# Kernel tuning notes

Hardware: AMD Instinct MI355X
Metric: run time of the kernel (lower is better)

## Reference

```python
import jax, jax.numpy as jnp
import numpy as np

B, R, C, H, W = 8, 4, 64, 128, 128
RF, E = 256, 8
C2 = 2 * C
K = 3


def setup_inputs() -> dict:
    key = jax.random.key(0)
    ks = jax.random.split(key, 8)
    return {
        "x": jax.random.normal(ks[0], (B, C, H, W), jnp.float32),
        "routing": jax.random.normal(ks[1], (B, R, RF), jnp.float32),
        # nn.Linear(routing_features, num_experts)
        "routing_W": jax.random.normal(ks[2], (RF, E), jnp.float32) * 0.05,
        "routing_b": jnp.zeros((E,), jnp.float32),
        # CondConv2d expert weights: (E, Cout, Cin, k, k)
        "W1": jax.random.normal(ks[3], (E, C2, C, K, K), jnp.float32) * 0.04,
        "prelu_a": jnp.float32(0.25),  # PReLU single shared parameter
        "W2": jax.random.normal(ks[4], (E, C, C2, K, K), jnp.float32) * 0.03,
        # self-routing Linear(2*in_features, num_experts)
        "sr_W": jax.random.normal(ks[5], (C2, E), jnp.float32) * 0.08,
        "sr_b": jnp.zeros((E,), jnp.float32),
        # conv_output: Conv2d(in_features, 1, kernel_size=1) with bias
        "Wout": jax.random.normal(ks[6], (1, C), jnp.float32) * 0.1,
        "bout": jnp.zeros((1,), jnp.float32),
    }


def _prelu(x, a):
    return jnp.where(x >= 0, x, a * x)


def _cond_conv(x, rw, Wexp):
    # x: (B,Cin,H,W); rw: (B,E); Wexp: (E,Cout,Cin,k,k)
    # per-sample mixed kernel, then per-sample conv (vmap over batch)
    w = jnp.einsum('be,eoikl->boikl', rw, Wexp)
    def one(xi, wi):
        return jax.lax.conv_general_dilated(
            xi[None], wi, window_strides=(1, 1), padding=[(1, 1), (1, 1)])[0]
    return jax.vmap(one)(x, w)


def reference(x, routing, routing_W, routing_b, W1, prelu_a, W2, sr_W, sr_b, Wout, bout):
    rw = jax.nn.sigmoid(routing @ routing_W + routing_b)  # (B,R,E)
    rw = jnp.transpose(rw, (1, 0, 2))                     # (R,B,E)

    def per_head(rw_r):
        xc = _prelu(_cond_conv(x, rw_r, W1), prelu_a)      # (B,C2,H,W)
        pooled = xc.mean(axis=(2, 3))                      # adaptive_avg_pool2d(.,1)
        srw = pooled @ sr_W + sr_b                         # no sigmoid (per source)
        xc2 = _prelu(_cond_conv(xc, srw, W2), prelu_a)     # (B,C,H,W)
        out = jnp.einsum('bchw,oc->bohw', xc2, Wout)       # 1x1 conv
        return out + bout[None, :, None, None]             # (B,1,H,W)

    res = jax.vmap(per_head)(rw)                           # (R,B,1,H,W)
    return jnp.transpose(res[:, :, 0], (1, 0, 2, 3))       # (B,R,H,W)
```

## Files before the change

### kernel.cpp

```cpp
#include <hip/hip_runtime.h>
#include <stdint.h>


typedef _Float16 f16_t;
typedef _Float16 f16x8 __attribute__((ext_vector_type(8)));
typedef _Float16 f16x4 __attribute__((ext_vector_type(4)));
typedef float    f32x4 __attribute__((ext_vector_type(4)));

#define B_   8
#define R_   4
#define C_   64
#define C2_  128
#define H_   128
#define W_   128
#define E_   8
#define RF_  256
#define WP_  130
#define HP_  130

__device__ __forceinline__ f32x4 mfma16(f16x8 a, f16x8 b, f32x4 c) {
  return __builtin_amdgcn_mfma_f32_16x16x32_f16(a, b, c, 0, 0, 0);
}

__device__ __forceinline__ void gl16(const f16_t* g, f16_t* l) {
  __builtin_amdgcn_global_load_lds(
      (const __attribute__((address_space(1))) unsigned int*)(const void*)g,
      (__attribute__((address_space(3))) unsigned int*)(void*)l, 16, 0, 0);
}

__device__ __host__ __forceinline__ int sig(int n) { return (n ^ (n >> 2)) & 3; }

__global__ void k_rw(const float* __restrict__ routing, const float* __restrict__ rW,
                     const float* __restrict__ rB, float* __restrict__ rw,
                     float* __restrict__ pooled4) {
  int t = threadIdx.x;
  #pragma unroll
  for (int i = 0; i < 16; ++i) pooled4[i*256 + t] = 0.f;
  int e = t & 7, b = (t >> 3) & 7, r = t >> 6;
  float acc = rB[e];
  for (int f = 0; f < RF_; ++f)
    acc += routing[(b*R_ + r)*RF_ + f] * rW[f*E_ + e];
  rw[(r*B_ + b)*E_ + e] = 1.0f / (1.0f + __expf(-acc));
}

__global__ void k_zero(f16_t* __restrict__ xbt, f16_t* __restrict__ xct) {
  const f16x8 z = {0,0,0,0,0,0,0,0};
  int t = blockIdx.x*256 + threadIdx.x;
  if (t < 16640) {
    int ch = t & 7, u = t >> 3;
    int pix = u % 130; u /= 130;
    int rs = u & 1, b = u >> 1;
    *(f16x8*)&xbt[((size_t)(b*HP_ + rs*129)*WP_ + pix)*C_ + ch*8] = z;
    return;
  }
  t -= 16640;
  if (t < 33280) {
    int ch = t & 15, u = t >> 4;
    int pix = u % 130; u /= 130;
    int rs = u & 1, b = u >> 1;
    *(f16x8*)&xct[((size_t)(b*HP_ + rs*129)*WP_ + pix)*C2_ + ch*8] = z;
    return;
  }
  t -= 33280;
  if (t < 32768) {
    int ch = t & 15, u = t >> 4;
    int hp = (u & 127) + 1; u >>= 7;
    int cs = u & 1, b = u >> 1;
    *(f16x8*)&xct[((size_t)(b*HP_ + hp)*WP_ + cs*129)*C2_ + ch*8] = z;
  }
}

__global__ void k_xt(const float* __restrict__ x, f16_t* __restrict__ xbt) {
  int wh = blockIdx.x, h = blockIdx.y, b = blockIdx.z;
  int t = threadIdx.x;
  int w0 = wh * 64;
  __shared__ float tile[64][65];
  #pragma unroll
  for (int rep = 0; rep < 16; ++rep) {
    int idx = rep*256 + t;
    int c = idx >> 6, w = idx & 63;
    tile[c][w] = x[((size_t)(b*C_ + c)*H_ + h)*W_ + w0 + w];
  }
  __syncthreads();
  #pragma unroll
  for (int rep = 0; rep < 16; ++rep) {
    int idx = rep*256 + t;
    int w = idx >> 6, c = idx & 63;
    xbt[((size_t)(b*HP_ + h + 1)*WP_ + (w0 + w + 1))*C_ + c] = (f16_t)tile[c][w];
  }
  if (t < 64) {
    if (wh == 0) xbt[((size_t)(b*HP_ + h + 1)*WP_ + 0)*C_ + t]   = (f16_t)0.0f;
    else         xbt[((size_t)(b*HP_ + h + 1)*WP_ + 129)*C_ + t] = (f16_t)0.0f;
  }
}

__global__ void k_mix1(const float* __restrict__ rw, const float* __restrict__ W1,
                       f16_t* __restrict__ w1m) {
  int gid = blockIdx.x*256 + threadIdx.x;
  int cq4 = gid & 15;
  int s   = (gid >> 4) % 9;
  int t2  = (gid >> 4) / 9;
  int co  = t2 & 127;
  int rb  = t2 >> 7;
  float o0=0.f,o1=0.f,o2=0.f,o3=0.f;
  #pragma unroll
  for (int e = 0; e < E_; ++e) {
    float rv = rw[rb*E_ + e];
    const float* wp = W1 + (size_t)((e*C2_ + co)*C_ + cq4*4)*9 + s;
    o0 += rv*wp[0]; o1 += rv*wp[9]; o2 += rv*wp[18]; o3 += rv*wp[27];
  }
  f16x4 pk; pk[0]=(f16_t)o0; pk[1]=(f16_t)o1; pk[2]=(f16_t)o2; pk[3]=(f16_t)o3;
  int coh = co >> 6, co6 = co & 63;
  int cb  = cq4 >> 3;
  int cqu = (cq4 >> 1) & 3;
  int off = (cq4 & 1) * 4;
  size_t row = ((size_t)(rb*2 + coh)*2 + cb)*64 + co6;
  *(f16x4*)&w1m[row*288 + (size_t)(s*4 + (cqu ^ sig(co6)))*8 + off] = pk;
}

__global__ void k_mix2(const float* __restrict__ pooled_r, const float* __restrict__ srW,
                       const float* __restrict__ srb, const float* __restrict__ W2,
                       f16_t* __restrict__ w2m) {
  __shared__ float sw[64];
  int t = threadIdx.x;
  if (t < 64) {
    int b = t >> 3, e = t & 7;
    float acc = srb[e];
    for (int c = 0; c < C2_; ++c)
      acc += pooled_r[b*C2_ + c] * (1.0f/16384.0f) * srW[c*E_ + e];
    sw[t] = acc;
  }
  __syncthreads();
  int gid = blockIdx.x*256 + t;
  int c2q = gid & 31;
  int s   = (gid >> 5) % 9;
  int t2  = (gid >> 5) / 9;
  int co  = t2 & 63;
  int b   = t2 >> 6;
  float o0=0.f,o1=0.f,o2=0.f,o3=0.f;
  #pragma unroll
  for (int e = 0; e < E_; ++e) {
    float rv = sw[b*E_ + e];
    const float* wp = W2 + (size_t)((e*C_ + co)*C2_ + c2q*4)*9 + s;
    o0 += rv*wp[0]; o1 += rv*wp[9]; o2 += rv*wp[18]; o3 += rv*wp[27];
  }
  f16x4 pk; pk[0]=(f16_t)o0; pk[1]=(f16_t)o1; pk[2]=(f16_t)o2; pk[3]=(f16_t)o3;
  int it  = c2q >> 3;
  int cqu = (c2q >> 1) & 3;
  int off = (c2q & 1) * 4;
  size_t row = ((size_t)b*4 + it)*64 + co;
  *(f16x4*)&w2m[row*288 + (size_t)(s*4 + (cqu ^ sig(co)))*8 + off] = pk;
}

__global__ __launch_bounds__(256, 2) void k_conv1(
    const f16_t* __restrict__ xbt, const f16_t* __restrict__ w1m,
    const float* __restrict__ pa, f16_t* __restrict__ xct,
    float* __restrict__ pooled_r, int r)
{
  const int bx = blockIdx.x;
  const int b = bx & 7, h0 = (bx >> 3) << 1;
  const int coh = blockIdx.y;
  const int tid = threadIdx.x;
  const int lane = tid & 63;
  const int wid = tid >> 6;
  const int wrow = wid >> 1, wph = wid & 1;
  const int l15 = lane & 15, l4 = lane >> 4;
  __shared__ __align__(16) f16_t lA[64*288];
  __shared__ __align__(16) f16_t lB[2080*8];

  const int xorA = (l4 ^ sig(l15)) << 4;
  int bbase[3];
  #pragma unroll
  for (int dw = 0; dw < 3; ++dw) {
    int P0 = wph*64 + dw + l15;
    bbase[dw] = P0*64 + ((l4 ^ sig(P0)) << 4);
  }

  const f32x4 vzero = {0.f,0.f,0.f,0.f};
  f32x4 acc[4][4];
  #pragma unroll
  for (int i=0;i<4;++i)
    #pragma unroll
    for (int j=0;j<4;++j) acc[i][j] = vzero;

  const int rb = r*B_ + b;
  const f16_t* w1base = w1m + ((size_t)(rb*2 + coh)*2)*64*288;
  const f16_t* xb = xbt + ((size_t)(b*HP_ + h0))*WP_*C_;

  for (int cb = 0; cb < 2; ++cb) {
    __syncthreads();
    #pragma unroll
    for (int k = 0; k < 9; ++k) {
      int u = k*256 + tid;
      gl16(w1base + (size_t)cb*64*288 + (size_t)u*8, &lA[u*8]);
    }
    #pragma unroll
    for (int k = 0; k < 8; ++k) {
      int u = k*256 + tid;
      int row = u / 520, rem = u - row*520;
      int pix = rem >> 2, cq = (rem & 3) ^ sig(pix);
      gl16(xb + ((size_t)row*WP_ + pix)*C_ + cb*32 + cq*8, &lB[u*8]);
    }
    if (tid < 32) {
      int u = 2048 + tid;
      int rem = u - 1560;
      int pix = rem >> 2, cq = (rem & 3) ^ sig(pix);
      gl16(xb + ((size_t)3*WP_ + pix)*C_ + cb*32 + cq*8, &lB[u*8]);
    }
    __syncthreads();
    __builtin_amdgcn_s_setprio(1);
    #pragma unroll
    for (int dh = 0; dh < 3; ++dh) {
      #pragma unroll
      for (int dw = 0; dw < 3; ++dw) {
        const int s = dh*3 + dw;
        f16x8 af[4], bf[4];
        #pragma unroll
        for (int fm = 0; fm < 4; ++fm)
          af[fm] = *(const f16x8*)((const char*)lA + (fm*16 + l15)*576 + s*64 + xorA);
        #pragma unroll
        for (int fn = 0; fn < 4; ++fn)
          bf[fn] = *(const f16x8*)((const char*)lB + (wrow + dh)*8320 + bbase[dw] + fn*1024);
        #pragma unroll
        for (int fm = 0; fm < 4; ++fm)
          #pragma unroll
          for (int fn = 0; fn < 4; ++fn)
            acc[fm][fn] = mfma16(af[fm], bf[fn], acc[fm][fn]);
      }
    }
    __builtin_amdgcn_s_setprio(0);
  }

  const float a = pa[0];
  float ps[4][4];
  #pragma unroll
  for (int fm=0;fm<4;++fm)
    #pragma unroll
    for (int j=0;j<4;++j) ps[fm][j] = 0.f;
  #pragma unroll
  for (int fm = 0; fm < 4; ++fm)
    #pragma unroll
    for (int fn = 0; fn < 4; ++fn)
      #pragma unroll
      for (int j = 0; j < 4; ++j) {
        float v = acc[fm][fn][j];
        v = (v >= 0.f) ? v : a*v;
        acc[fm][fn][j] = v;
        ps[fm][j] += v;
      }
  #pragma unroll
  for (int fm = 0; fm < 4; ++fm)
    #pragma unroll
    for (int j = 0; j < 4; ++j) {
      float s = ps[fm][j];
      s += __shfl_xor(s, 1, 64);
      s += __shfl_xor(s, 2, 64);
      s += __shfl_xor(s, 4, 64);
      s += __shfl_xor(s, 8, 64);
      ps[fm][j] = s;
    }
  __syncthreads();
  f16_t* lso = lA;
  float* lps = (float*)lB;
  const int prow = wrow*128 + wph*64;
  #pragma unroll
  for (int fm = 0; fm < 4; ++fm)
    #pragma unroll
    for (int fn = 0; fn < 4; ++fn) {
      f16x4 pk;
      #pragma unroll
      for (int j = 0; j < 4; ++j) pk[j] = (f16_t)acc[fm][fn][j];
      *(f16x4*)&lso[(prow + fn*16 + l15)*72 + fm*16 + l4*4] = pk;
    }
  if (l15 == 0) {
    #pragma unroll
    for (int fm = 0; fm < 4; ++fm)
      #pragma unroll
      for (int j = 0; j < 4; ++j)
        lps[wid*64 + fm*16 + l4*4 + j] = ps[fm][j];
  }
  __syncthreads();
  #pragma unroll
  for (int p = 0; p < 8; ++p) {
    int i = p*256 + tid;
    int pl = i >> 3, q = i & 7;
    int row = pl >> 7, pix = pl & 127;
    uint4 v = *(const uint4*)&lso[pl*72 + q*8];
    *(uint4*)(xct + ((size_t)(b*HP_ + h0 + row + 1)*WP_ + pix + 1)*C2_ + coh*64 + q*8) = v;
  }
  if (tid < 64) {
    float s = lps[tid] + lps[64 + tid] + lps[128 + tid] + lps[192 + tid];
    atomicAdd(&pooled_r[b*C2_ + coh*64 + tid], s);
  }
}

__global__ __launch_bounds__(256, 2) void k_conv2(
    const f16_t* __restrict__ xct, const f16_t* __restrict__ w2m,
    const float* __restrict__ pa, const float* __restrict__ Wout,
    const float* __restrict__ bout, float* __restrict__ out, int r)
{
  const int bx = blockIdx.x;
  const int b = bx & 7, h0 = (bx >> 3) << 1;
  const int tid = threadIdx.x;
  const int lane = tid & 63;
  const int wid = tid >> 6;
  const int wrow = wid >> 1, wph = wid & 1;
  const int l15 = lane & 15, l4 = lane >> 4;
  __shared__ __align__(16) f16_t lA[64*288];
  __shared__ __align__(16) f16_t lB[2080*8];

  const int xorA = (l4 ^ sig(l15)) << 4;
  int bbase[3];
  #pragma unroll
  for (int dw = 0; dw < 3; ++dw) {
    int P0 = wph*64 + dw + l15;
    bbase[dw] = P0*64 + ((l4 ^ sig(P0)) << 4);
  }

  const f32x4 vzero = {0.f,0.f,0.f,0.f};
  f32x4 acc[4][4];
  #pragma unroll
  for (int i=0;i<4;++i)
    #pragma unroll
    for (int j=0;j<4;++j) acc[i][j] = vzero;

  const f16_t* w2base = w2m + (size_t)b*4*64*288;
  const f16_t* xb = xct + ((size_t)(b*HP_ + h0))*WP_*C2_;

  for (int it = 0; it < 4; ++it) {
    __syncthreads();
    #pragma unroll
    for (int k = 0; k < 9; ++k) {
      int u = k*256 + tid;
      gl16(w2base + (size_t)it*64*288 + (size_t)u*8, &lA[u*8]);
    }
    #pragma unroll
    for (int k = 0; k < 8; ++k) {
      int u = k*256 + tid;
      int row = u / 520, rem = u - row*520;
      int pix = rem >> 2, cq = (rem & 3) ^ sig(pix);
      gl16(xb + ((size_t)row*WP_ + pix)*C2_ + it*32 + cq*8, &lB[u*8]);
    }
    if (tid < 32) {
      int u = 2048 + tid;
      int rem = u - 1560;
      int pix = rem >> 2, cq = (rem & 3) ^ sig(pix);
      gl16(xb + ((size_t)3*WP_ + pix)*C2_ + it*32 + cq*8, &lB[u*8]);
    }
    __syncthreads();
    __builtin_amdgcn_s_setprio(1);
    #pragma unroll
    for (int dh = 0; dh < 3; ++dh) {
      #pragma unroll
      for (int dw = 0; dw < 3; ++dw) {
        const int s = dh*3 + dw;
        f16x8 af[4], bf[4];
        #pragma unroll
        for (int fm = 0; fm < 4; ++fm)
          af[fm] = *(const f16x8*)((const char*)lA + (fm*16 + l15)*576 + s*64 + xorA);
        #pragma unroll
        for (int fn = 0; fn < 4; ++fn)
          bf[fn] = *(const f16x8*)((const char*)lB + (wrow + dh)*8320 + bbase[dw] + fn*1024);
        #pragma unroll
        for (int fm = 0; fm < 4; ++fm)
          #pragma unroll
          for (int fn = 0; fn < 4; ++fn)
            acc[fm][fn] = mfma16(af[fm], bf[fn], acc[fm][fn]);
      }
    }
    __builtin_amdgcn_s_setprio(0);
  }

  const float a  = pa[0];
  const float bo = bout[0];
  float wr_[4][4];
  #pragma unroll
  for (int fm = 0; fm < 4; ++fm)
    #pragma unroll
    for (int j = 0; j < 4; ++j)
      wr_[fm][j] = Wout[fm*16 + l4*4 + j];
  float* orow = out + ((size_t)((b*R_ + r)*H_ + h0 + wrow))*W_;
  #pragma unroll
  for (int fn = 0; fn < 4; ++fn) {
    float s = 0.f;
    #pragma unroll
    for (int fm = 0; fm < 4; ++fm)
      #pragma unroll
      for (int j = 0; j < 4; ++j) {
        float v = acc[fm][fn][j];
        v = (v >= 0.f) ? v : a*v;
        s += wr_[fm][j]*v;
      }
    s += __shfl_xor(s, 16, 64);
    s += __shfl_xor(s, 32, 64);
    if (lane < 16)
      orow[wph*64 + fn*16 + lane] = s + bo;
  }
}

extern "C" void kernel_launch(void* const* d_in, const int* in_sizes, int n_in,
                              void* d_out, int out_size, void* d_ws, size_t ws_size,
                              hipStream_t stream) {
  (void)in_sizes; (void)n_in; (void)out_size; (void)ws_size;
  const float* x       = (const float*)d_in[0];
  const float* routing = (const float*)d_in[1];
  const float* rW      = (const float*)d_in[2];
  const float* rB      = (const float*)d_in[3];
  const float* W1      = (const float*)d_in[4];
  const float* pa      = (const float*)d_in[5];
  const float* W2      = (const float*)d_in[6];
  const float* srW     = (const float*)d_in[7];
  const float* srb     = (const float*)d_in[8];
  const float* Wout    = (const float*)d_in[9];
  const float* bout    = (const float*)d_in[10];
  float* out = (float*)d_out;

  char* ws = (char*)d_ws;
  size_t off = 0;
  f16_t* xbt = (f16_t*)(ws + off); off += (size_t)B_*HP_*WP_*C_*2;
  f16_t* w1m = (f16_t*)(ws + off); off += (size_t)8192*288*2;
  f16_t* xct = (f16_t*)(ws + off); off += (size_t)B_*HP_*WP_*C2_*2;
  f16_t* w2m = (f16_t*)(ws + off); off += (size_t)2048*288*2;
  float* rw     = (float*)(ws + off); off += (size_t)R_*B_*E_*4;
  float* pooled = (float*)(ws + off); off += (size_t)R_*B_*C2_*4;

  k_rw  <<<1, 256, 0, stream>>>(routing, rW, rB, rw, pooled);
  k_zero<<<323, 256, 0, stream>>>(xbt, xct);
  k_xt  <<<dim3(2, H_, B_), 256, 0, stream>>>(x, xbt);
  k_mix1<<<2304, 256, 0, stream>>>(rw, W1, w1m);
  for (int r = 0; r < R_; ++r) {
    float* pooled_r = pooled + (size_t)r*B_*C2_;
    k_conv1<<<dim3(512, 2), 256, 0, stream>>>(xbt, w1m, pa, xct, pooled_r, r);
    k_mix2 <<<576, 256, 0, stream>>>(pooled_r, srW, srb, W2, w2m);
    k_conv2<<<dim3(512), 256, 0, stream>>>(xct, w2m, pa, Wout, bout, out, r);
  }
}
```

Baseline: 293.2 us.

## Batch the four routing heads into single conv and mix launches

The per-head loop of conv1, mix2 and conv2 launches is replaced by one launch of each kernel, with the head index taken from an extra grid dimension. Each head gets its own copy of the intermediate activation buffer and the mixed weight buffer, and the zero-padding kernel now clears the halos of all four copies. This aims to cut launch overhead and the serialization between heads, and to fill the GPU with more blocks at once. The cost is four times the intermediate workspace and more cache pressure. The code falls back to the old per-head loop if the workspace is too small.

Result: faster. 242.8 us (-17.2%).

```diff
diff --git a/kernel.cpp b/kernel.cpp
--- a/kernel.cpp
+++ b/kernel.cpp
@@ -43,7 +43,8 @@
   rw[(r*B_ + b)*E_ + e] = 1.0f / (1.0f + __expf(-acc));
 }
 
-__global__ void k_zero(f16_t* __restrict__ xbt, f16_t* __restrict__ xct) {
+__global__ void k_zero(f16_t* __restrict__ xbt, f16_t* __restrict__ xct,
+                       size_t xct_stride) {
   const f16x8 z = {0,0,0,0,0,0,0,0};
   int t = blockIdx.x*256 + threadIdx.x;
   if (t < 16640) {
@@ -54,19 +55,21 @@
     return;
   }
   t -= 16640;
-  if (t < 33280) {
+  if (t < 133120) {
     int ch = t & 15, u = t >> 4;
     int pix = u % 130; u /= 130;
-    int rs = u & 1, b = u >> 1;
-    *(f16x8*)&xct[((size_t)(b*HP_ + rs*129)*WP_ + pix)*C2_ + ch*8] = z;
+    int rs = u & 1; u >>= 1;
+    int b = u & 7, r = u >> 3;
+    *(f16x8*)&xct[(size_t)r*xct_stride + ((size_t)(b*HP_ + rs*129)*WP_ + pix)*C2_ + ch*8] = z;
     return;
   }
-  t -= 33280;
-  if (t < 32768) {
+  t -= 133120;
+  if (t < 131072) {
     int ch = t & 15, u = t >> 4;
     int hp = (u & 127) + 1; u >>= 7;
-    int cs = u & 1, b = u >> 1;
-    *(f16x8*)&xct[((size_t)(b*HP_ + hp)*WP_ + cs*129)*C2_ + ch*8] = z;
+    int cs = u & 1; u >>= 1;
+    int b = u & 7, r = u >> 3;
+    *(f16x8*)&xct[(size_t)r*xct_stride + ((size_t)(b*HP_ + hp)*WP_ + cs*129)*C2_ + ch*8] = z;
   }
 }
 
@@ -118,9 +121,12 @@
   *(f16x4*)&w1m[row*288 + (size_t)(s*4 + (cqu ^ sig(co6)))*8 + off] = pk;
 }
 
-__global__ void k_mix2(const float* __restrict__ pooled_r, const float* __restrict__ srW,
+__global__ void k_mix2(const float* __restrict__ pooled, const float* __restrict__ srW,
                        const float* __restrict__ srb, const float* __restrict__ W2,
-                       f16_t* __restrict__ w2m) {
+                       f16_t* __restrict__ w2m, size_t w2m_stride, int r0) {
+  const int r = r0 + blockIdx.y;
+  const float* pooled_r = pooled + (size_t)r*B_*C2_;
+  f16_t* w2m_r = w2m + (size_t)r*w2m_stride;
   __shared__ float sw[64];
   int t = threadIdx.x;
   if (t < 64) {
@@ -149,17 +155,20 @@
   int cqu = (c2q >> 1) & 3;
   int off = (c2q & 1) * 4;
   size_t row = ((size_t)b*4 + it)*64 + co;
-  *(f16x4*)&w2m[row*288 + (size_t)(s*4 + (cqu ^ sig(co)))*8 + off] = pk;
+  *(f16x4*)&w2m_r[row*288 + (size_t)(s*4 + (cqu ^ sig(co)))*8 + off] = pk;
 }
 
 __global__ __launch_bounds__(256, 2) void k_conv1(
     const f16_t* __restrict__ xbt, const f16_t* __restrict__ w1m,
-    const float* __restrict__ pa, f16_t* __restrict__ xct,
-    float* __restrict__ pooled_r, int r)
+    const float* __restrict__ pa, f16_t* __restrict__ xct, size_t xct_stride,
+    float* __restrict__ pooled, int r0)
 {
   const int bx = blockIdx.x;
   const int b = bx & 7, h0 = (bx >> 3) << 1;
   const int coh = blockIdx.y;
+  const int r = r0 + blockIdx.z;
+  f16_t* xct_r = xct + (size_t)r*xct_stride;
+  float* pooled_r = pooled + (size_t)r*B_*C2_;
   const int tid = threadIdx.x;
   const int lane = tid & 63;
   const int wid = tid >> 6;
@@ -286,7 +295,7 @@
     int pl = i >> 3, q = i & 7;
     int row = pl >> 7, pix = pl & 127;
     uint4 v = *(const uint4*)&lso[pl*72 + q*8];
-    *(uint4*)(xct + ((size_t)(b*HP_ + h0 + row + 1)*WP_ + pix + 1)*C2_ + coh*64 + q*8) = v;
+    *(uint4*)(xct_r + ((size_t)(b*HP_ + h0 + row + 1)*WP_ + pix + 1)*C2_ + coh*64 + q*8) = v;
   }
   if (tid < 64) {
     float s = lps[tid] + lps[64 + tid] + lps[128 + tid] + lps[192 + tid];
@@ -295,12 +304,14 @@
 }
 
 __global__ __launch_bounds__(256, 2) void k_conv2(
-    const f16_t* __restrict__ xct, const f16_t* __restrict__ w2m,
+    const f16_t* __restrict__ xct, size_t xct_stride,
+    const f16_t* __restrict__ w2m, size_t w2m_stride,
     const float* __restrict__ pa, const float* __restrict__ Wout,
-    const float* __restrict__ bout, float* __restrict__ out, int r)
+    const float* __restrict__ bout, float* __restrict__ out, int r0)
 {
   const int bx = blockIdx.x;
   const int b = bx & 7, h0 = (bx >> 3) << 1;
+  const int r = r0 + blockIdx.y;
   const int tid = threadIdx.x;
   const int lane = tid & 63;
   const int wid = tid >> 6;
@@ -324,8 +335,8 @@
     #pragma unroll
     for (int j=0;j<4;++j) acc[i][j] = vzero;
 
-  const f16_t* w2base = w2m + (size_t)b*4*64*288;
-  const f16_t* xb = xct + ((size_t)(b*HP_ + h0))*WP_*C2_;
+  const f16_t* w2base = w2m + (size_t)r*w2m_stride + (size_t)b*4*64*288;
+  const f16_t* xb = xct + (size_t)r*xct_stride + ((size_t)(b*HP_ + h0))*WP_*C2_;
 
   for (int it = 0; it < 4; ++it) {
     __syncthreads();
@@ -401,7 +412,7 @@
 extern "C" void kernel_launch(void* const* d_in, const int* in_sizes, int n_in,
                               void* d_out, int out_size, void* d_ws, size_t ws_size,
                               hipStream_t stream) {
-  (void)in_sizes; (void)n_in; (void)out_size; (void)ws_size;
+  (void)in_sizes; (void)n_in; (void)out_size;
   const float* x       = (const float*)d_in[0];
   const float* routing = (const float*)d_in[1];
   const float* rW      = (const float*)d_in[2];
@@ -415,23 +426,36 @@
   const float* bout    = (const float*)d_in[10];
   float* out = (float*)d_out;
 
+  const size_t xct_one = (size_t)B_*HP_*WP_*C2_;
+  const size_t w2m_one = (size_t)2048*288;
+  const size_t need_fused = 17305600ull + 4718592ull + 4*xct_one*2 + 4*w2m_one*2 + 32768ull;
+  const bool fused = (ws_size >= need_fused);
+  const int ncopies = fused ? 4 : 1;
+  const size_t xs = fused ? xct_one : 0;
+  const size_t ws2 = fused ? w2m_one : 0;
+
   char* ws = (char*)d_ws;
   size_t off = 0;
   f16_t* xbt = (f16_t*)(ws + off); off += (size_t)B_*HP_*WP_*C_*2;
   f16_t* w1m = (f16_t*)(ws + off); off += (size_t)8192*288*2;
-  f16_t* xct = (f16_t*)(ws + off); off += (size_t)B_*HP_*WP_*C2_*2;
-  f16_t* w2m = (f16_t*)(ws + off); off += (size_t)2048*288*2;
+  f16_t* xct = (f16_t*)(ws + off); off += xct_one*2*ncopies;
+  f16_t* w2m = (f16_t*)(ws + off); off += w2m_one*2*ncopies;
   float* rw     = (float*)(ws + off); off += (size_t)R_*B_*E_*4;
   float* pooled = (float*)(ws + off); off += (size_t)R_*B_*C2_*4;
 
   k_rw  <<<1, 256, 0, stream>>>(routing, rW, rB, rw, pooled);
-  k_zero<<<323, 256, 0, stream>>>(xbt, xct);
+  k_zero<<<1097, 256, 0, stream>>>(xbt, xct, xs);
   k_xt  <<<dim3(2, H_, B_), 256, 0, stream>>>(x, xbt);
   k_mix1<<<2304, 256, 0, stream>>>(rw, W1, w1m);
-  for (int r = 0; r < R_; ++r) {
-    float* pooled_r = pooled + (size_t)r*B_*C2_;
-    k_conv1<<<dim3(512, 2), 256, 0, stream>>>(xbt, w1m, pa, xct, pooled_r, r);
-    k_mix2 <<<576, 256, 0, stream>>>(pooled_r, srW, srb, W2, w2m);
-    k_conv2<<<dim3(512), 256, 0, stream>>>(xct, w2m, pa, Wout, bout, out, r);
-  }
-}
+  if (fused) {
+    k_conv1<<<dim3(512, 2, 4), 256, 0, stream>>>(xbt, w1m, pa, xct, xs, pooled, 0);
+    k_mix2 <<<dim3(576, 4), 256, 0, stream>>>(pooled, srW, srb, W2, w2m, ws2, 0);
+    k_conv2<<<dim3(512, 4), 256, 0, stream>>>(xct, xs, w2m, ws2, pa, Wout, bout, out, 0);
+  } else {
+    for (int r = 0; r < R_; ++r) {
+      k_conv1<<<dim3(512, 2, 1), 256, 0, stream>>>(xbt, w1m, pa, xct, xs, pooled, r);
+      k_mix2 <<<dim3(576, 1), 256, 0, stream>>>(pooled, srW, srb, W2, w2m, ws2, r);
+      k_conv2<<<dim3(512, 1), 256, 0, stream>>>(xct, xs, w2m, ws2, pa, Wout, bout, out, r);
+    }
+  }
+}
```
